# Performance work log

Measured on AMD Instinct MI355X. Metric: run time of the kernel, lower is better.

## Reference

```python
import jax, jax.numpy as jnp
import numpy as np

B, F, H, W = 2, 512, 192, 192
T = 8
NEAR, FAR = 0.5, 100.0
EPS = 1e-8


def setup_inputs() -> dict:
    key = jax.random.key(0)
    k1, k2, k3, k4, k5 = jax.random.split(key, 5)
    # triangles in NDC: xy in [-1,1], z (depth) in [NEAR, FAR)
    center = jax.random.uniform(k1, (B, F, 1, 2), minval=-0.9, maxval=0.9)
    offset = jax.random.uniform(k2, (B, F, 3, 2), minval=-0.15, maxval=0.15)
    xy = center + offset                                      # [B,F,3,2]
    z = (jax.random.uniform(k3, (B, F, 1, 1), minval=2.0, maxval=8.0)
         + jax.random.uniform(k5, (B, F, 3, 1), minval=0.0, maxval=0.2))
    faces = jnp.concatenate([xy, z], axis=-1)                 # [B,F,3,3]
    textures = jax.random.normal(k4, (B, F, 3, T))            # per-vertex features
    return {"faces": faces, "textures": textures}


def _rasterize_maps(faces):
    # faces: [B,F,3,3] -> face_index_map [B,H,W] int32, weight_map [B,H,W,3], depth_map [B,H,W]
    dt = faces.dtype
    px = ((2.0 * (jnp.arange(W, dtype=dt) + 0.5) - W) / W)[None, None, None, :]  # [1,1,1,W]
    py = ((2.0 * (jnp.arange(H, dtype=dt) + 0.5) - H) / H)[None, None, :, None]  # [1,1,H,1]
    x = faces[..., 0][..., None, None]  # [B,F,3,1,1]
    y = faces[..., 1][..., None, None]
    z = faces[..., 2][..., None, None]
    x0, x1, x2 = x[:, :, 0], x[:, :, 1], x[:, :, 2]  # [B,F,1,1]
    y0, y1, y2 = y[:, :, 0], y[:, :, 1], y[:, :, 2]
    z0, z1, z2 = z[:, :, 0], z[:, :, 1], z[:, :, 2]
    det = (x1 - x0) * (y2 - y0) - (x2 - x0) * (y1 - y0)
    ok = jnp.abs(det) > EPS
    inv_det = jnp.where(ok, det, 1.0)
    inv_det = 1.0 / inv_det
    # screen-space barycentric weights, [B,F,H,W]
    w0 = ((x1 - px) * (y2 - py) - (x2 - px) * (y1 - py)) * inv_det
    w1 = ((x2 - px) * (y0 - py) - (x0 - px) * (y2 - py)) * inv_det
    w2 = 1.0 - w0 - w1
    inside = (w0 >= 0.0) & (w1 >= 0.0) & (w2 >= 0.0) & ok
    # perspective-correct depth: 1 / sum_k w_k / z_k
    inv_depth = w0 / z0 + w1 / z1 + w2 / z2
    depth = jnp.where(inv_depth > EPS, 1.0 / jnp.maximum(inv_depth, EPS), FAR)
    valid = inside & (depth >= NEAR) & (depth <= FAR)
    cand = jnp.where(valid, depth, FAR)            # [B,F,H,W]
    best = jnp.argmin(cand, axis=1)                # z-buffer winner, [B,H,W]
    take = lambda a: jnp.take_along_axis(a, best[:, None], axis=1)[:, 0]
    min_depth = take(cand)
    covered = min_depth < FAR
    face_index_map = jnp.where(covered, best, -1).astype(jnp.int32)
    weight_map = jnp.where(covered[..., None],
                           jnp.stack([take(w0), take(w1), take(w2)], axis=-1), 0.0)
    depth_map = jnp.where(covered, min_depth, FAR)
    return face_index_map, weight_map, depth_map


def reference(faces, textures):
    fim, wmap, dmap = _rasterize_maps(faces)
    Bp = faces.shape[0]
    idx = jnp.maximum(fim, 0).reshape(Bp, H * W)
    # gather winning face's per-vertex features: [B,HW,3,T]
    tex = jnp.take_along_axis(textures, idx[:, :, None, None], axis=1)
    feat = jnp.einsum('bpk,bpkt->bpt', wmap.reshape(Bp, H * W, 3), tex).reshape(Bp, H, W, T)
    mask = (fim >= 0).astype(feat.dtype)[..., None]
    feature_map = jnp.concatenate([feat, mask], axis=-1)   # [B,H,W,T+1]
    feature = jnp.transpose(feature_map, (0, 3, 1, 2))     # [B,T+1,H,W]
    return feature, fim, dmap
```

## Files before the change

### kernel.cpp

```cpp
#include <hip/hip_runtime.h>
#include <hip/hip_bf16.h>


namespace {
constexpr int BB = 2, FF = 512, HH = 192, WW = 192, TT = 8;
constexpr int TILE = 16;
constexpr int HWSZ = HH * WW;
constexpr int RAW = FF * 9;
constexpr float NEARF = 0.5f, FARF = 100.0f, EPSF = 1e-8f;
}

__global__ __launch_bounds__(256) void raster_fused_kernel(
    const float* __restrict__ faces,
    const float* __restrict__ textures,
    float* __restrict__ out)
{
#pragma clang fp contract(off)
  __shared__ float sraw[RAW];
  __shared__ float sface[FF * 12];
  __shared__ int s_count;
  __shared__ unsigned short s_list[FF];

  const int tx = threadIdx.x, ty = threadIdx.y;
  const int tid = ty * TILE + tx;
  const int bx = blockIdx.x, by = blockIdx.y, b = blockIdx.z;

  if (tid == 0) s_count = 0;

  {
    const float4* src = (const float4*)(faces + (size_t)b * RAW);
    float4* dst = (float4*)sraw;
    for (int i = tid; i < RAW / 4; i += 256) dst[i] = src[i];
  }
  __syncthreads();

  const float px_lo = (2.0f * ((float)(bx * TILE) + 0.5f) - (float)WW) / (float)WW;
  const float px_hi = (2.0f * ((float)(bx * TILE + TILE - 1) + 0.5f) - (float)WW) / (float)WW;
  const float py_lo = (2.0f * ((float)(by * TILE) + 0.5f) - (float)HH) / (float)HH;
  const float py_hi = (2.0f * ((float)(by * TILE + TILE - 1) + 0.5f) - (float)HH) / (float)HH;

  for (int f = tid; f < FF; f += 256) {
    const float* fp = sraw + f * 9;
    float x0 = fp[0], y0 = fp[1], z0 = fp[2];
    float x1 = fp[3], y1 = fp[4], z1 = fp[5];
    float x2 = fp[6], y2 = fp[7], z2 = fp[8];
    float det = (x1 - x0) * (y2 - y0) - (x2 - x0) * (y1 - y0);
    bool ok = fabsf(det) > EPSF;
    float invdet = 1.0f / (ok ? det : 1.0f);
    float* dst = sface + f * 12;
    dst[0] = x0; dst[1] = y0; dst[2] = x1; dst[3] = y1;
    dst[4] = x2; dst[5] = y2; dst[6] = invdet; dst[7] = 1.0f / z0;
    dst[8] = 1.0f / z1; dst[9] = 1.0f / z2;
    if (ok) {
      float xmn = fminf(x0, fminf(x1, x2)), xmx = fmaxf(x0, fmaxf(x1, x2));
      float ymn = fminf(y0, fminf(y1, y2)), ymx = fmaxf(y0, fmaxf(y1, y2));
      if (xmx >= px_lo && xmn <= px_hi && ymx >= py_lo && ymn <= py_hi) {
        int slot = atomicAdd(&s_count, 1);
        s_list[slot] = (unsigned short)f;
      }
    }
  }
  __syncthreads();

  const int w = bx * TILE + tx;
  const int h = by * TILE + ty;
  const float px = (2.0f * ((float)w + 0.5f) - (float)WW) / (float)WW;
  const float py = (2.0f * ((float)h + 0.5f) - (float)HH) / (float)HH;

  float best = FARF;
  int bestf = 0;
  float bw0 = 0.0f, bw1 = 0.0f, bw2 = 0.0f;
  const int cnt = s_count;

  if (cnt > 0) {
    int fnext = s_list[0];
    float4 r0 = *(const float4*)(sface + fnext * 12);
    float4 r1 = *(const float4*)(sface + fnext * 12 + 4);
    float2 r2 = *(const float2*)(sface + fnext * 12 + 8);
    for (int i = 0; i < cnt; ++i) {
      const float4 c0 = r0; const float4 c1 = r1; const float2 c2 = r2;
      const int fcur = fnext;
      if (i + 1 < cnt) {
        fnext = s_list[i + 1];
        r0 = *(const float4*)(sface + fnext * 12);
        r1 = *(const float4*)(sface + fnext * 12 + 4);
        r2 = *(const float2*)(sface + fnext * 12 + 8);
      }
      float dx0 = c0.x - px, dy0 = c0.y - py;
      float dx1 = c0.z - px, dy1 = c0.w - py;
      float dx2 = c1.x - px, dy2 = c1.y - py;
      float w0 = (dx1 * dy2 - dx2 * dy1) * c1.z;
      float w1 = (dx2 * dy0 - dx0 * dy2) * c1.z;
      float w2 = 1.0f - w0 - w1;
      if (w0 >= 0.0f && w1 >= 0.0f && w2 >= 0.0f) {
        float invd = w0 * c1.w + w1 * c2.x + w2 * c2.y;
        if (invd > EPSF) {
          float d = 1.0f / invd;
          if (d >= NEARF && d <= FARF && d < best) {
            best = d; bestf = fcur;
            bw0 = w0; bw1 = w1; bw2 = w2;
          }
        }
      }
    }
  }

  const bool covered = best < FARF;
  const size_t pix = (size_t)h * WW + w;
  float* featp = out + (size_t)b * 9 * HWSZ + pix;
  if (covered) {
    const float4* tp = (const float4*)(textures + (size_t)(b * FF + bestf) * 3 * TT);
    float4 t0 = tp[0], t1 = tp[1];
    float4 t2 = tp[2], t3 = tp[3];
    float4 t4 = tp[4], t5 = tp[5];
    const float* v0 = (const float*)&t0;
    float a0[8] = {t0.x, t0.y, t0.z, t0.w, t1.x, t1.y, t1.z, t1.w};
    float a1[8] = {t2.x, t2.y, t2.z, t2.w, t3.x, t3.y, t3.z, t3.w};
    float a2[8] = {t4.x, t4.y, t4.z, t4.w, t5.x, t5.y, t5.z, t5.w};
    (void)v0;
    #pragma unroll
    for (int t = 0; t < TT; ++t) {
      float v = bw0 * a0[t] + bw1 * a1[t];
      v = v + bw2 * a2[t];
      featp[(size_t)t * HWSZ] = v;
    }
    featp[(size_t)TT * HWSZ] = 1.0f;
  } else {
    #pragma unroll
    for (int t = 0; t < TT + 1; ++t) featp[(size_t)t * HWSZ] = 0.0f;
  }

  const size_t fim_base = (size_t)BB * 9 * HWSZ;
  const size_t dmap_base = fim_base + (size_t)BB * HWSZ;
  out[fim_base + (size_t)b * HWSZ + pix] = covered ? (float)bestf : -1.0f;
  out[dmap_base + (size_t)b * HWSZ + pix] = best;
}

extern "C" void kernel_launch(void* const* d_in, const int* in_sizes, int n_in,
                              void* d_out, int out_size, void* d_ws, size_t ws_size,
                              hipStream_t stream) {
  const float* faces = (const float*)d_in[0];
  const float* textures = (const float*)d_in[1];
  float* out = (float*)d_out;
  dim3 grid(WW / TILE, HH / TILE, BB);
  dim3 block(TILE, TILE, 1);
  hipLaunchKernelGGL(raster_fused_kernel, grid, block, 0, stream,
                     faces, textures, out);
}
```

Before: 62.60 us.

## Split rasterizer into a global face-binning pass and a per-tile render pass

A new kernel computes per-face setup once per batch: edge data, inverse determinant and inverse depths. It bins each face into screen tiles by its pixel bounding box, using global atomics to build per-tile face lists in workspace memory. The render kernel then loads only its tile's candidate faces into a compacted shared array, with the face id stored in the record. This drops the redundant per-block loading and setup of all 512 faces and the list indirection in the inner loop. The cost is a second launch with a serial dependency and a binning kernel that runs only two blocks.

```diff
diff --git a/kernel.cpp b/kernel.cpp
--- a/kernel.cpp
+++ b/kernel.cpp
@@ -1,64 +1,90 @@
 #include <hip/hip_runtime.h>
-#include <hip/hip_bf16.h>
 
 
 namespace {
 constexpr int BB = 2, FF = 512, HH = 192, WW = 192, TT = 8;
 constexpr int TILE = 16;
+constexpr int NTX = WW / TILE, NTY = HH / TILE, NTILES = NTX * NTY;
 constexpr int HWSZ = HH * WW;
 constexpr int RAW = FF * 9;
 constexpr float NEARF = 0.5f, FARF = 100.0f, EPSF = 1e-8f;
+constexpr size_t WS_RECS = 0;
+constexpr size_t WS_COUNTS = 49152;
+constexpr size_t WS_LISTS = 50304;
 }
 
-__global__ __launch_bounds__(256) void raster_fused_kernel(
+__global__ __launch_bounds__(512) void bin_faces_kernel(
     const float* __restrict__ faces,
+    float* __restrict__ recs,
+    int* __restrict__ counts,
+    unsigned short* __restrict__ lists)
+{
+#pragma clang fp contract(off)
+  const int b = blockIdx.x;
+  const int f = threadIdx.x;
+  int* cnts = counts + b * NTILES;
+  if (f < NTILES) cnts[f] = 0;
+  __syncthreads();
+
+  const float* fp = faces + (size_t)b * RAW + (size_t)f * 9;
+  const float x0 = fp[0], y0 = fp[1], z0 = fp[2];
+  const float x1 = fp[3], y1 = fp[4], z1 = fp[5];
+  const float x2 = fp[6], y2 = fp[7], z2 = fp[8];
+  const float det = (x1 - x0) * (y2 - y0) - (x2 - x0) * (y1 - y0);
+  const bool ok = fabsf(det) > EPSF;
+  const float invdet = 1.0f / (ok ? det : 1.0f);
+
+  float4* dst = (float4*)(recs + ((size_t)b * FF + f) * 12);
+  dst[0] = make_float4(x0, y0, x1, y1);
+  dst[1] = make_float4(x2, y2, invdet, 1.0f / z0);
+  dst[2] = make_float4(1.0f / z1, 1.0f / z2, 0.0f, 0.0f);
+  if (!ok) return;
+
+  const float xmn = fminf(x0, fminf(x1, x2)), xmx = fmaxf(x0, fmaxf(x1, x2));
+  const float ymn = fminf(y0, fminf(y1, y2)), ymx = fmaxf(y0, fmaxf(y1, y2));
+  const int wlo = max(0, (int)floorf((xmn + 1.0f) * (0.5f * WW) - 0.5f));
+  const int whi = min(WW - 1, (int)ceilf((xmx + 1.0f) * (0.5f * WW) - 0.5f));
+  const int hlo = max(0, (int)floorf((ymn + 1.0f) * (0.5f * HH) - 0.5f));
+  const int hhi = min(HH - 1, (int)ceilf((ymx + 1.0f) * (0.5f * HH) - 0.5f));
+  if (whi < wlo || hhi < hlo) return;
+  const int tx0 = wlo / TILE, tx1 = whi / TILE;
+  const int ty0 = hlo / TILE, ty1 = hhi / TILE;
+  for (int ty = ty0; ty <= ty1; ++ty) {
+    for (int tx = tx0; tx <= tx1; ++tx) {
+      const int t = ty * NTX + tx;
+      const int slot = atomicAdd(&cnts[t], 1);
+      lists[((size_t)b * NTILES + t) * FF + slot] = (unsigned short)f;
+    }
+  }
+}
+
+__global__ __launch_bounds__(256) void render_kernel(
+    const float* __restrict__ recs,
+    const int* __restrict__ counts,
+    const unsigned short* __restrict__ lists,
     const float* __restrict__ textures,
     float* __restrict__ out)
 {
 #pragma clang fp contract(off)
-  __shared__ float sraw[RAW];
   __shared__ float sface[FF * 12];
-  __shared__ int s_count;
-  __shared__ unsigned short s_list[FF];
 
   const int tx = threadIdx.x, ty = threadIdx.y;
   const int tid = ty * TILE + tx;
   const int bx = blockIdx.x, by = blockIdx.y, b = blockIdx.z;
+  const int tile = by * NTX + bx;
 
-  if (tid == 0) s_count = 0;
+  const int cnt = counts[b * NTILES + tile];
+  const unsigned short* lst = lists + ((size_t)b * NTILES + tile) * FF;
 
-  {
-    const float4* src = (const float4*)(faces + (size_t)b * RAW);
-    float4* dst = (float4*)sraw;
-    for (int i = tid; i < RAW / 4; i += 256) dst[i] = src[i];
-  }
-  __syncthreads();
-
-  const float px_lo = (2.0f * ((float)(bx * TILE) + 0.5f) - (float)WW) / (float)WW;
-  const float px_hi = (2.0f * ((float)(bx * TILE + TILE - 1) + 0.5f) - (float)WW) / (float)WW;
-  const float py_lo = (2.0f * ((float)(by * TILE) + 0.5f) - (float)HH) / (float)HH;
-  const float py_hi = (2.0f * ((float)(by * TILE + TILE - 1) + 0.5f) - (float)HH) / (float)HH;
-
-  for (int f = tid; f < FF; f += 256) {
-    const float* fp = sraw + f * 9;
-    float x0 = fp[0], y0 = fp[1], z0 = fp[2];
-    float x1 = fp[3], y1 = fp[4], z1 = fp[5];
-    float x2 = fp[6], y2 = fp[7], z2 = fp[8];
-    float det = (x1 - x0) * (y2 - y0) - (x2 - x0) * (y1 - y0);
-    bool ok = fabsf(det) > EPSF;
-    float invdet = 1.0f / (ok ? det : 1.0f);
-    float* dst = sface + f * 12;
-    dst[0] = x0; dst[1] = y0; dst[2] = x1; dst[3] = y1;
-    dst[4] = x2; dst[5] = y2; dst[6] = invdet; dst[7] = 1.0f / z0;
-    dst[8] = 1.0f / z1; dst[9] = 1.0f / z2;
-    if (ok) {
-      float xmn = fminf(x0, fminf(x1, x2)), xmx = fmaxf(x0, fmaxf(x1, x2));
-      float ymn = fminf(y0, fminf(y1, y2)), ymx = fmaxf(y0, fmaxf(y1, y2));
-      if (xmx >= px_lo && xmn <= px_hi && ymx >= py_lo && ymn <= py_hi) {
-        int slot = atomicAdd(&s_count, 1);
-        s_list[slot] = (unsigned short)f;
-      }
-    }
+  for (int i = tid; i < cnt; i += 256) {
+    const int f = lst[i];
+    const float4* src = (const float4*)(recs + ((size_t)b * FF + f) * 12);
+    float4 r0 = src[0];
+    float4 r1 = src[1];
+    float4 r2 = src[2];
+    r2.z = (float)f;
+    float4* dst = (float4*)(sface + i * 12);
+    dst[0] = r0; dst[1] = r1; dst[2] = r2;
   }
   __syncthreads();
 
@@ -70,21 +96,18 @@
   float best = FARF;
   int bestf = 0;
   float bw0 = 0.0f, bw1 = 0.0f, bw2 = 0.0f;
-  const int cnt = s_count;
 
   if (cnt > 0) {
-    int fnext = s_list[0];
-    float4 r0 = *(const float4*)(sface + fnext * 12);
-    float4 r1 = *(const float4*)(sface + fnext * 12 + 4);
-    float2 r2 = *(const float2*)(sface + fnext * 12 + 8);
+    float4 r0 = *(const float4*)(sface + 0);
+    float4 r1 = *(const float4*)(sface + 4);
+    float4 r2 = *(const float4*)(sface + 8);
     for (int i = 0; i < cnt; ++i) {
-      const float4 c0 = r0; const float4 c1 = r1; const float2 c2 = r2;
-      const int fcur = fnext;
+      const float4 c0 = r0; const float4 c1 = r1; const float4 c2 = r2;
       if (i + 1 < cnt) {
-        fnext = s_list[i + 1];
-        r0 = *(const float4*)(sface + fnext * 12);
-        r1 = *(const float4*)(sface + fnext * 12 + 4);
-        r2 = *(const float2*)(sface + fnext * 12 + 8);
+        const float* p = sface + (size_t)(i + 1) * 12;
+        r0 = *(const float4*)(p);
+        r1 = *(const float4*)(p + 4);
+        r2 = *(const float4*)(p + 8);
       }
       float dx0 = c0.x - px, dy0 = c0.y - py;
       float dx1 = c0.z - px, dy1 = c0.w - py;
@@ -97,7 +120,7 @@
         if (invd > EPSF) {
           float d = 1.0f / invd;
           if (d >= NEARF && d <= FARF && d < best) {
-            best = d; bestf = fcur;
+            best = d; bestf = (int)c2.z;
             bw0 = w0; bw1 = w1; bw2 = w2;
           }
         }
@@ -113,11 +136,9 @@
     float4 t0 = tp[0], t1 = tp[1];
     float4 t2 = tp[2], t3 = tp[3];
     float4 t4 = tp[4], t5 = tp[5];
-    const float* v0 = (const float*)&t0;
     float a0[8] = {t0.x, t0.y, t0.z, t0.w, t1.x, t1.y, t1.z, t1.w};
     float a1[8] = {t2.x, t2.y, t2.z, t2.w, t3.x, t3.y, t3.z, t3.w};
     float a2[8] = {t4.x, t4.y, t4.z, t4.w, t5.x, t5.y, t5.z, t5.w};
-    (void)v0;
     #pragma unroll
     for (int t = 0; t < TT; ++t) {
       float v = bw0 * a0[t] + bw1 * a1[t];
@@ -139,11 +160,17 @@
 extern "C" void kernel_launch(void* const* d_in, const int* in_sizes, int n_in,
                               void* d_out, int out_size, void* d_ws, size_t ws_size,
                               hipStream_t stream) {
+  (void)in_sizes; (void)n_in; (void)out_size; (void)ws_size;
   const float* faces = (const float*)d_in[0];
   const float* textures = (const float*)d_in[1];
   float* out = (float*)d_out;
-  dim3 grid(WW / TILE, HH / TILE, BB);
-  dim3 block(TILE, TILE, 1);
-  hipLaunchKernelGGL(raster_fused_kernel, grid, block, 0, stream,
-                     faces, textures, out);
+
+  float* recs = (float*)((char*)d_ws + WS_RECS);
+  int* counts = (int*)((char*)d_ws + WS_COUNTS);
+  unsigned short* lists = (unsigned short*)((char*)d_ws + WS_LISTS);
+
+  hipLaunchKernelGGL(bin_faces_kernel, dim3(BB), dim3(512), 0, stream,
+                     faces, recs, counts, lists);
+  hipLaunchKernelGGL(render_kernel, dim3(NTX, NTY, BB), dim3(TILE, TILE), 0, stream,
+                     recs, counts, lists, textures, out);
 }
```

Result: slower. 66.33 us (+6.0%).

## Compact binned faces contiguously in LDS with wave ballot and enlarge tile

Applied to the files above, without the earlier changes.

Faces are read directly from global memory and no longer staged raw in shared memory. Faces that pass the tile bounding-box test are written into a dense, contiguous LDS array, with the face id packed into the record. Slots are reserved with one atomic per wave via ballot and popcount. This removes the index-list indirection and the per-thread LDS atomics in the hot per-pixel loop. The tile also grows from 16x16 to 16x24 (384 threads), which cuts the grid to 192 blocks and makes each tile's candidate list longer.

```diff
diff --git a/kernel.cpp b/kernel.cpp
--- a/kernel.cpp
+++ b/kernel.cpp
@@ -1,69 +1,68 @@
 #include <hip/hip_runtime.h>
-#include <hip/hip_bf16.h>
 
 
 namespace {
 constexpr int BB = 2, FF = 512, HH = 192, WW = 192, TT = 8;
-constexpr int TILE = 16;
+constexpr int TW = 16, TH = 24;
+constexpr int NTHR = TW * TH;
 constexpr int HWSZ = HH * WW;
-constexpr int RAW = FF * 9;
 constexpr float NEARF = 0.5f, FARF = 100.0f, EPSF = 1e-8f;
 }
 
-__global__ __launch_bounds__(256) void raster_fused_kernel(
+__global__ __launch_bounds__(NTHR) void raster_fused_kernel(
     const float* __restrict__ faces,
     const float* __restrict__ textures,
     float* __restrict__ out)
 {
 #pragma clang fp contract(off)
-  __shared__ float sraw[RAW];
   __shared__ float sface[FF * 12];
   __shared__ int s_count;
-  __shared__ unsigned short s_list[FF];
 
   const int tx = threadIdx.x, ty = threadIdx.y;
-  const int tid = ty * TILE + tx;
+  const int tid = ty * TW + tx;
+  const int lane = tid & 63;
   const int bx = blockIdx.x, by = blockIdx.y, b = blockIdx.z;
 
   if (tid == 0) s_count = 0;
 
-  {
-    const float4* src = (const float4*)(faces + (size_t)b * RAW);
-    float4* dst = (float4*)sraw;
-    for (int i = tid; i < RAW / 4; i += 256) dst[i] = src[i];
-  }
+  const float px_lo = (2.0f * ((float)(bx * TW) + 0.5f) - (float)WW) / (float)WW;
+  const float px_hi = (2.0f * ((float)(bx * TW + TW - 1) + 0.5f) - (float)WW) / (float)WW;
+  const float py_lo = (2.0f * ((float)(by * TH) + 0.5f) - (float)HH) / (float)HH;
+  const float py_hi = (2.0f * ((float)(by * TH + TH - 1) + 0.5f) - (float)HH) / (float)HH;
+
   __syncthreads();
 
-  const float px_lo = (2.0f * ((float)(bx * TILE) + 0.5f) - (float)WW) / (float)WW;
-  const float px_hi = (2.0f * ((float)(bx * TILE + TILE - 1) + 0.5f) - (float)WW) / (float)WW;
-  const float py_lo = (2.0f * ((float)(by * TILE) + 0.5f) - (float)HH) / (float)HH;
-  const float py_hi = (2.0f * ((float)(by * TILE + TILE - 1) + 0.5f) - (float)HH) / (float)HH;
-
-  for (int f = tid; f < FF; f += 256) {
-    const float* fp = sraw + f * 9;
-    float x0 = fp[0], y0 = fp[1], z0 = fp[2];
-    float x1 = fp[3], y1 = fp[4], z1 = fp[5];
-    float x2 = fp[6], y2 = fp[7], z2 = fp[8];
-    float det = (x1 - x0) * (y2 - y0) - (x2 - x0) * (y1 - y0);
-    bool ok = fabsf(det) > EPSF;
-    float invdet = 1.0f / (ok ? det : 1.0f);
-    float* dst = sface + f * 12;
-    dst[0] = x0; dst[1] = y0; dst[2] = x1; dst[3] = y1;
-    dst[4] = x2; dst[5] = y2; dst[6] = invdet; dst[7] = 1.0f / z0;
-    dst[8] = 1.0f / z1; dst[9] = 1.0f / z2;
+  for (int f = tid; f < FF; f += NTHR) {
+    const float* fp = faces + (size_t)b * (FF * 9) + (size_t)f * 9;
+    const float x0 = fp[0], y0 = fp[1], z0 = fp[2];
+    const float x1 = fp[3], y1 = fp[4], z1 = fp[5];
+    const float x2 = fp[6], y2 = fp[7], z2 = fp[8];
+    const float det = (x1 - x0) * (y2 - y0) - (x2 - x0) * (y1 - y0);
+    const bool ok = fabsf(det) > EPSF;
+    const float invdet = 1.0f / (ok ? det : 1.0f);
+    bool pass = false;
     if (ok) {
-      float xmn = fminf(x0, fminf(x1, x2)), xmx = fmaxf(x0, fmaxf(x1, x2));
-      float ymn = fminf(y0, fminf(y1, y2)), ymx = fmaxf(y0, fmaxf(y1, y2));
-      if (xmx >= px_lo && xmn <= px_hi && ymx >= py_lo && ymn <= py_hi) {
-        int slot = atomicAdd(&s_count, 1);
-        s_list[slot] = (unsigned short)f;
-      }
+      const float xmn = fminf(x0, fminf(x1, x2)), xmx = fmaxf(x0, fmaxf(x1, x2));
+      const float ymn = fminf(y0, fminf(y1, y2)), ymx = fmaxf(y0, fmaxf(y1, y2));
+      pass = (xmx >= px_lo && xmn <= px_hi && ymx >= py_lo && ymn <= py_hi);
+    }
+    const unsigned long long m = __ballot(pass);
+    const int wtotal = __popcll(m);
+    int wbase = 0;
+    if (lane == 0 && wtotal) wbase = atomicAdd(&s_count, wtotal);
+    wbase = __shfl(wbase, 0);
+    if (pass) {
+      const int slot = wbase + __popcll(m & ((1ull << lane) - 1ull));
+      float* dst = sface + slot * 12;
+      ((float4*)dst)[0] = make_float4(x0, y0, x1, y1);
+      ((float4*)dst)[1] = make_float4(x2, y2, invdet, 1.0f / z0);
+      ((float4*)dst)[2] = make_float4(1.0f / z1, 1.0f / z2, (float)f, 0.0f);
     }
   }
   __syncthreads();
 
-  const int w = bx * TILE + tx;
-  const int h = by * TILE + ty;
+  const int w = bx * TW + tx;
+  const int h = by * TH + ty;
   const float px = (2.0f * ((float)w + 0.5f) - (float)WW) / (float)WW;
   const float py = (2.0f * ((float)h + 0.5f) - (float)HH) / (float)HH;
 
@@ -73,18 +72,16 @@
   const int cnt = s_count;
 
   if (cnt > 0) {
-    int fnext = s_list[0];
-    float4 r0 = *(const float4*)(sface + fnext * 12);
-    float4 r1 = *(const float4*)(sface + fnext * 12 + 4);
-    float2 r2 = *(const float2*)(sface + fnext * 12 + 8);
+    float4 r0 = *(const float4*)(sface + 0);
+    float4 r1 = *(const float4*)(sface + 4);
+    float4 r2 = *(const float4*)(sface + 8);
     for (int i = 0; i < cnt; ++i) {
-      const float4 c0 = r0; const float4 c1 = r1; const float2 c2 = r2;
-      const int fcur = fnext;
+      const float4 c0 = r0; const float4 c1 = r1; const float4 c2 = r2;
       if (i + 1 < cnt) {
-        fnext = s_list[i + 1];
-        r0 = *(const float4*)(sface + fnext * 12);
-        r1 = *(const float4*)(sface + fnext * 12 + 4);
-        r2 = *(const float2*)(sface + fnext * 12 + 8);
+        const float* p = sface + (size_t)(i + 1) * 12;
+        r0 = *(const float4*)(p);
+        r1 = *(const float4*)(p + 4);
+        r2 = *(const float4*)(p + 8);
       }
       float dx0 = c0.x - px, dy0 = c0.y - py;
       float dx1 = c0.z - px, dy1 = c0.w - py;
@@ -97,7 +94,7 @@
         if (invd > EPSF) {
           float d = 1.0f / invd;
           if (d >= NEARF && d <= FARF && d < best) {
-            best = d; bestf = fcur;
+            best = d; bestf = (int)c2.z;
             bw0 = w0; bw1 = w1; bw2 = w2;
           }
         }
@@ -113,11 +110,9 @@
     float4 t0 = tp[0], t1 = tp[1];
     float4 t2 = tp[2], t3 = tp[3];
     float4 t4 = tp[4], t5 = tp[5];
-    const float* v0 = (const float*)&t0;
     float a0[8] = {t0.x, t0.y, t0.z, t0.w, t1.x, t1.y, t1.z, t1.w};
     float a1[8] = {t2.x, t2.y, t2.z, t2.w, t3.x, t3.y, t3.z, t3.w};
     float a2[8] = {t4.x, t4.y, t4.z, t4.w, t5.x, t5.y, t5.z, t5.w};
-    (void)v0;
     #pragma unroll
     for (int t = 0; t < TT; ++t) {
       float v = bw0 * a0[t] + bw1 * a1[t];
@@ -139,11 +134,12 @@
 extern "C" void kernel_launch(void* const* d_in, const int* in_sizes, int n_in,
                               void* d_out, int out_size, void* d_ws, size_t ws_size,
                               hipStream_t stream) {
+  (void)in_sizes; (void)n_in; (void)out_size; (void)d_ws; (void)ws_size;
   const float* faces = (const float*)d_in[0];
   const float* textures = (const float*)d_in[1];
   float* out = (float*)d_out;
-  dim3 grid(WW / TILE, HH / TILE, BB);
-  dim3 block(TILE, TILE, 1);
+  dim3 grid(WW / TW, HH / TH, BB);
+  dim3 block(TW, TH, 1);
   hipLaunchKernelGGL(raster_fused_kernel, grid, block, 0, stream,
                      faces, textures, out);
 }
```

Result: no change. 62.20 us (-0.6%).
